# Kernel tuning notes

Measured on AMD Instinct MI355X. Metric: run time of the kernel, lower is better.

Reference implementation:

```python
import jax, jax.numpy as jnp
from jax import lax
import numpy as np

B, CIN, COUT, N, H, W = 16, 64, 64, 8, 128, 128


def setup_inputs() -> dict:
    key = jax.random.key(0)
    ks = jax.random.split(key, 6)
    s = 0.05
    return {
        "x": jax.random.normal(ks[0], (B, CIN, H, W), dtype=jnp.float32),
        "condition": jax.random.normal(ks[1], (B, CIN), dtype=jnp.float32),
        "filt_w": jax.random.normal(ks[2], (N, COUT, CIN, 3, 3), dtype=jnp.float32) * s,
        "filt_b": jax.random.normal(ks[3], (N, COUT), dtype=jnp.float32) * s,
        "sel_w": jax.random.normal(ks[4], (N, CIN), dtype=jnp.float32) * s,
        "sel_b": jax.random.normal(ks[5], (N,), dtype=jnp.float32) * s,
    }


def reference(x, condition, filt_w, filt_b, sel_w, sel_b):
    b = x.shape[0]
    # condition selector: Linear(in_channels -> num_conditions) + softmax
    logits = condition.reshape(b, -1) @ sel_w.T + sel_b          # [B, N]
    weights = jax.nn.softmax(logits, axis=-1)                    # [B, N]

    n, cout, cin, kh, kw = filt_w.shape
    # Run all N branch convs in ONE conv by stacking filters on the output-channel axis.
    kern = filt_w.reshape(n * cout, cin, kh, kw)
    y = lax.conv_general_dilated(
        x, kern, window_strides=(1, 1), padding="SAME",
        dimension_numbers=("NCHW", "OIHW", "NCHW"))              # [B, N*COUT, H, W]
    h, w = y.shape[-2], y.shape[-1]
    y = y.reshape(b, n, cout, h, w) + filt_b.reshape(1, n, cout, 1, 1)
    # softmax-gated sum over the N branches
    out = jnp.einsum("bn,bnohw->bohw", weights, y)
    return out
```

## Files before the change

### kernel.cpp

```cpp
#include <hip/hip_runtime.h>
#include <stdint.h>

#define BATCH 16
#define CIN   64
#define COUT  64
#define NBR   8
#define HH    128
#define WW    128
#define XBH   130
#define XBW   130
#define PSTR  68
#define NTILES 1024

typedef __attribute__((ext_vector_type(8)))  short short8;
typedef __attribute__((ext_vector_type(16))) float f32x16;

__device__ __forceinline__ unsigned int f2bf_hi(float f) {
    union { float f; uint32_t u; } v; v.f = f;
    return (v.u + 0x8000u) >> 16;
}
__device__ __forceinline__ unsigned short f2bf(float f) {
    union { float f; uint32_t u; } v; v.f = f;
    uint32_t u = v.u;
    return (unsigned short)((u + 0x7FFFu + ((u >> 16) & 1u)) >> 16);
}
__device__ __forceinline__ short8 gld_frag(const unsigned short* p) {
    union { uint4 u; short8 s; } t;
    t.u = *(const uint4*)p;
    return t.s;
}
__device__ __forceinline__ short8 lds_frag(const unsigned short* p) {
    union { uint2 u[2]; short8 s; } t;
    t.u[0] = *(const uint2*)p;
    t.u[1] = *(const uint2*)(p + 4);
    return t.s;
}
__device__ __forceinline__ void gload_lds16(const unsigned short* g, unsigned short* l) {
    __builtin_amdgcn_global_load_lds(
        (const __attribute__((address_space(1))) unsigned int*)g,
        (__attribute__((address_space(3))) unsigned int*)l, 16, 0, 0);
}

__global__ __launch_bounds__(256)
void k_pc(const float* __restrict__ cond,
          const float* __restrict__ sel_w,
          const float* __restrict__ sel_b,
          const float* __restrict__ filt_w,
          const float* __restrict__ filt_b,
          const float* __restrict__ x,
          unsigned short* __restrict__ wfilt,
          float* __restrict__ cbias,
          unsigned short* __restrict__ xb) {
    __shared__ float4 lw4[NBR * 144];
    __shared__ float lg[NBR];
    const int tid = threadIdx.x;

    if (blockIdx.x < NTILES) {
        float* lw = (float*)lw4;
        const int blk = blockIdx.x;
        const int b = blk >> 6, o = blk & 63;

        const float4* src4 = (const float4*)filt_w;
        #pragma unroll
        for (int i = tid; i < NBR * 144; i += 256)
            lw4[i] = src4[((i / 144) * COUT + o) * 144 + (i % 144)];

        {
            const int lane = tid & 63, w = tid >> 6;
            const float c0 = cond[b * CIN + lane];
            #pragma unroll
            for (int k = 0; k < 2; ++k) {
                const int n = w + k * 4;
                float p = c0 * sel_w[n * CIN + lane];
                #pragma unroll
                for (int off = 32; off > 0; off >>= 1)
                    p += __shfl_down(p, off, 64);
                if (lane == 0) lg[n] = p + sel_b[n];
            }
        }
        __syncthreads();

        float w8[NBR];
        {
            float m = -1e30f;
            #pragma unroll
            for (int n = 0; n < NBR; ++n) m = fmaxf(m, lg[n]);
            float s = 0.f;
            #pragma unroll
            for (int n = 0; n < NBR; ++n) { w8[n] = __expf(lg[n] - m); s += w8[n]; }
            const float inv = 1.f / s;
            #pragma unroll
            for (int n = 0; n < NBR; ++n) w8[n] *= inv;
        }

        #pragma unroll
        for (int idx = tid; idx < 576; idx += 256) {
            const int t = idx >> 6, c = idx & 63;
            float acc = 0.f;
            #pragma unroll
            for (int n = 0; n < NBR; ++n)
                acc += w8[n] * lw[n * 576 + c * 9 + t];
            wfilt[(((long)(b * 9 + t) * COUT + o) << 6) + c] = f2bf(acc);
        }
        if (tid == 0) {
            float ab = 0.f;
            #pragma unroll
            for (int n = 0; n < NBR; ++n) ab += w8[n] * filt_b[n * COUT + o];
            cbias[b * COUT + o] = ab;
        }
    } else {
        const int id = blockIdx.x - NTILES;
        const int hp = id % XBH;
        const int b  = id / XBH;
        unsigned short* dst = xb + (long)(b * XBH + hp) * XBW * PSTR;
        const bool zrow = (hp == 0) || (hp == XBH - 1);
        const int h = hp - 1;
        const long cs = (long)HH * WW;

        for (int t = tid; t < XBW * 8; t += 256) {
            const int wp = t >> 3, q = t & 7;
            uint4 v; v.x = v.y = v.z = v.w = 0u;
            if (!zrow && wp != 0 && wp != XBW - 1) {
                const float* px = x + (((long)(b * CIN + q * 8)) * HH + h) * WW + (wp - 1);
                v.x = f2bf_hi(px[0])      | (f2bf_hi(px[cs])     << 16);
                v.y = f2bf_hi(px[2 * cs]) | (f2bf_hi(px[3 * cs]) << 16);
                v.z = f2bf_hi(px[4 * cs]) | (f2bf_hi(px[5 * cs]) << 16);
                v.w = f2bf_hi(px[6 * cs]) | (f2bf_hi(px[7 * cs]) << 16);
            }
            unsigned short* dp = dst + wp * PSTR + q * 8;
            uint2 u0, u1;
            u0.x = v.x; u0.y = v.y; u1.x = v.z; u1.y = v.w;
            *(uint2*)dp       = u0;
            *(uint2*)(dp + 4) = u1;
            if (q == 7) {
                uint2 z; z.x = z.y = 0u;
                *(uint2*)(dst + wp * PSTR + 64) = z;
            }
        }
    }
}

#define RT 4
#define WT 32
#define SLABW 34
#define SLABR 6
#define ROWUS (SLABW * PSTR)
#define NCHUNK (SLABR * ROWUS / 8)

__global__ __launch_bounds__(256, 4)
void k_conv(const unsigned short* __restrict__ xb,
            const unsigned short* __restrict__ wfilt,
            const float* __restrict__ cbias,
            float* __restrict__ out) {
    __shared__ unsigned short lx[SLABR * ROWUS];

    const int b  = blockIdx.z;
    const int h0 = blockIdx.y * RT;
    const int w0 = blockIdx.x * WT;
    const int tid = threadIdx.x;

    const unsigned short* srcb = xb + ((long)(b * XBH + h0) * XBW + w0) * PSTR;
    #pragma unroll
    for (int k = 0; k < 7; ++k) {
        const int t = tid + k * 256;
        if (t < NCHUNK) {
            const int row = t / 289;
            const int rc  = t - row * 289;
            gload_lds16(srcb + (long)row * (XBW * PSTR) + rc * 8, lx + t * 8);
        }
    }

    const int lane = tid & 63;
    const int wave = tid >> 6;
    const int l31  = lane & 31;
    const int lh   = lane >> 5;
    const int wp   = wave & 1;
    const int wc   = wave >> 1;
    const int r0   = wp * 2;

    const unsigned short* wf = wfilt + (long)b * 9 * COUT * CIN + wc * 32 * CIN;

    short8 A[4];
    #pragma unroll
    for (int cc = 0; cc < 4; ++cc)
        A[cc] = gld_frag(wf + l31 * CIN + cc * 16 + lh * 8);

    f32x16 acc0, acc1;
    #pragma unroll
    for (int i = 0; i < 16; ++i) {
        const int m = (i & 3) + 8 * (i >> 2) + 4 * lh;
        const float bb = cbias[b * COUT + wc * 32 + m];
        acc0[i] = bb; acc1[i] = bb;
    }

    __syncthreads();

    #pragma unroll
    for (int tap = 0; tap < 9; ++tap) {
        short8 nA[4];
        if (tap < 8) {
            const unsigned short* wn = wf + (long)(tap + 1) * COUT * CIN;
            #pragma unroll
            for (int cc = 0; cc < 4; ++cc)
                nA[cc] = gld_frag(wn + l31 * CIN + cc * 16 + lh * 8);
        }
        const int kh = tap / 3, kw = tap % 3;
        #pragma unroll
        for (int cc = 0; cc < 4; ++cc) {
            const int kofs = cc * 16 + lh * 8;
            short8 b0 = lds_frag(&lx[((r0     + kh) * SLABW + l31 + kw) * PSTR + kofs]);
            short8 b1 = lds_frag(&lx[((r0 + 1 + kh) * SLABW + l31 + kw) * PSTR + kofs]);
            acc0 = __builtin_amdgcn_mfma_f32_32x32x16_bf16(A[cc], b0, acc0, 0, 0, 0);
            acc1 = __builtin_amdgcn_mfma_f32_32x32x16_bf16(A[cc], b1, acc1, 0, 0, 0);
        }
        #pragma unroll
        for (int cc = 0; cc < 4; ++cc) A[cc] = nA[cc];
    }

    #pragma unroll
    for (int pb = 0; pb < 2; ++pb) {
        const f32x16 v = pb == 0 ? acc0 : acc1;
        const int hrow = h0 + r0 + pb;
        float* op = out + (((long)(b * COUT + wc * 32) * HH + hrow) * WW + w0 + l31);
        #pragma unroll
        for (int i = 0; i < 16; ++i) {
            const int m = (i & 3) + 8 * (i >> 2) + 4 * lh;
            op[(long)m * HH * WW] = v[i];
        }
    }
}

extern "C" void kernel_launch(void* const* d_in, const int* in_sizes, int n_in,
                              void* d_out, int out_size, void* d_ws, size_t ws_size,
                              hipStream_t stream) {
    const float* x      = (const float*)d_in[0];
    const float* cond   = (const float*)d_in[1];
    const float* filt_w = (const float*)d_in[2];
    const float* filt_b = (const float*)d_in[3];
    const float* sel_w  = (const float*)d_in[4];
    const float* sel_b  = (const float*)d_in[5];
    float* out = (float*)d_out;

    float*          cbias = (float*)d_ws;
    unsigned short* wfilt = (unsigned short*)((char*)d_ws + 4096);
    unsigned short* xb    = (unsigned short*)((char*)d_ws + 4096 + 1179648);

    k_pc<<<NTILES + BATCH * XBH, 256, 0, stream>>>(cond, sel_w, sel_b, filt_w, filt_b, x,
                                                   wfilt, cbias, xb);

    dim3 grid(WW / WT, HH / RT, BATCH);
    k_conv<<<grid, 256, 0, stream>>>(xb, wfilt, cbias, out);
}
```

Before: 183.7 us.

## Transpose x rows through LDS with float4 loads and raise conv occupancy hint

The NCHW-to-padded-NHWC bf16 conversion blocks now read each input row with coalesced float4 loads, transpose it through shared memory (reusing the filter-mixing LDS buffer), and then write packed channel vectors. Before, each thread gathered scalars strided across channels. Fully zero padding rows now take an early-exit path. The conv kernel's launch bounds go from 4 to 5 blocks per SIMD, which may force register pressure or spills.

```diff
diff --git a/kernel.cpp b/kernel.cpp
--- a/kernel.cpp
+++ b/kernel.cpp
@@ -51,12 +51,13 @@
           unsigned short* __restrict__ wfilt,
           float* __restrict__ cbias,
           unsigned short* __restrict__ xb) {
-    __shared__ float4 lw4[NBR * 144];
-    __shared__ float lg[NBR];
+    __shared__ __align__(16) char smem[NBR * 144 * 16 + 64];
     const int tid = threadIdx.x;
 
     if (blockIdx.x < NTILES) {
-        float* lw = (float*)lw4;
+        float4* lw4 = (float4*)smem;
+        float*  lg  = (float*)(smem + NBR * 144 * 16);
+        float*  lw  = (float*)lw4;
         const int blk = blockIdx.x;
         const int b = blk >> 6, o = blk & 63;
 
@@ -113,23 +114,40 @@
         const int hp = id % XBH;
         const int b  = id / XBH;
         unsigned short* dst = xb + (long)(b * XBH + hp) * XBW * PSTR;
-        const bool zrow = (hp == 0) || (hp == XBH - 1);
+
+        if (hp == 0 || hp == XBH - 1) {
+            uint2 z; z.x = z.y = 0u;
+            for (int t = tid; t < XBW * PSTR / 4; t += 256)
+                *(uint2*)&dst[t * 4] = z;
+            return;
+        }
         const int h = hp - 1;
-        const long cs = (long)HH * WW;
+
+        unsigned short* lt = (unsigned short*)smem;
+
+        #pragma unroll
+        for (int k = 0; k < 8; ++k) {
+            const int u = tid + k * 256;
+            const int c = u >> 5;
+            const int j = u & 31;
+            const float4 v = *(const float4*)(x + ((long)(b * CIN + c) * HH + h) * WW + j * 4);
+            const int w = j * 4;
+            lt[(w    ) * 66 + c] = (unsigned short)f2bf_hi(v.x);
+            lt[(w + 1) * 66 + c] = (unsigned short)f2bf_hi(v.y);
+            lt[(w + 2) * 66 + c] = (unsigned short)f2bf_hi(v.z);
+            lt[(w + 3) * 66 + c] = (unsigned short)f2bf_hi(v.w);
+        }
+        __syncthreads();
 
         for (int t = tid; t < XBW * 8; t += 256) {
             const int wp = t >> 3, q = t & 7;
-            uint4 v; v.x = v.y = v.z = v.w = 0u;
-            if (!zrow && wp != 0 && wp != XBW - 1) {
-                const float* px = x + (((long)(b * CIN + q * 8)) * HH + h) * WW + (wp - 1);
-                v.x = f2bf_hi(px[0])      | (f2bf_hi(px[cs])     << 16);
-                v.y = f2bf_hi(px[2 * cs]) | (f2bf_hi(px[3 * cs]) << 16);
-                v.z = f2bf_hi(px[4 * cs]) | (f2bf_hi(px[5 * cs]) << 16);
-                v.w = f2bf_hi(px[6 * cs]) | (f2bf_hi(px[7 * cs]) << 16);
+            uint2 u0, u1;
+            u0.x = u0.y = u1.x = u1.y = 0u;
+            if (wp > 0 && wp < XBW - 1) {
+                const unsigned int* lp = (const unsigned int*)&lt[(wp - 1) * 66 + q * 8];
+                u0.x = lp[0]; u0.y = lp[1]; u1.x = lp[2]; u1.y = lp[3];
             }
             unsigned short* dp = dst + wp * PSTR + q * 8;
-            uint2 u0, u1;
-            u0.x = v.x; u0.y = v.y; u1.x = v.z; u1.y = v.w;
             *(uint2*)dp       = u0;
             *(uint2*)(dp + 4) = u1;
             if (q == 7) {
@@ -147,7 +165,7 @@
 #define ROWUS (SLABW * PSTR)
 #define NCHUNK (SLABR * ROWUS / 8)
 
-__global__ __launch_bounds__(256, 4)
+__global__ __launch_bounds__(256, 5)
 void k_conv(const unsigned short* __restrict__ xb,
             const unsigned short* __restrict__ wfilt,
             const float* __restrict__ cbias,
```

After: 173.8 us. -5.4%, faster.
